# Kernel tuning notes

Hardware: AMD Instinct MI355X
Metric: run time of the kernel (lower is better)

## Reference

```python
import jax, jax.numpy as jnp
import numpy as np

BN_EPS = 1e-5
K = 3  # k_size


def _unfold(x, k):
    # torch F.unfold with padding=k//2, stride=1, viewed as (B, C, k*k, H, W).
    # Kernel positions are row-major (i slow, j fast), matching torch layout.
    p = k // 2
    B, C, H, W = x.shape
    xp = jnp.pad(x, ((0, 0), (0, 0), (p, p), (p, p)))
    pats = jnp.stack([xp[:, :, i:i + H, j:j + W]
                      for i in range(k) for j in range(k)], axis=2)
    return pats  # (B, C, k*k, H, W)


def _conv1x1(x, w, b):
    # w: (C_out, C_in), x: (B, C_in, H, W)
    return jnp.einsum('oc,bchw->bohw', w, x) + b[None, :, None, None]


def _bn(x, gamma, beta, mean, var):
    inv = gamma / jnp.sqrt(var + BN_EPS)
    return x * inv[None, :, None, None] + (beta - mean * inv)[None, :, None, None]


def setup_inputs() -> dict:
    key = jax.random.key(0)
    ks = jax.random.split(key, 12)
    B, C, H, W = 8, 256, 64, 64
    s = lambda k_, *sh: jax.random.normal(k_, sh, dtype=jnp.float32) * 0.05
    return {
        'x': jax.random.normal(ks[0], (B, C, H, W), dtype=jnp.float32),
        # feature_embedding: Conv2d(C, C, 1) + BN
        'w_embed': s(ks[1], C, C), 'b_embed': jnp.zeros((C,), jnp.float32),
        'bn1_gamma': jnp.ones((C,), jnp.float32), 'bn1_beta': jnp.zeros((C,), jnp.float32),
        'bn1_mean': jnp.zeros((C,), jnp.float32), 'bn1_var': jnp.ones((C,), jnp.float32),
        # enhance: Conv2d(2C, C, 1) + BN
        'w_enh': s(ks[2], C, 2 * C), 'b_enh': jnp.zeros((C,), jnp.float32),
        'bn2_gamma': jnp.ones((C,), jnp.float32), 'bn2_beta': jnp.zeros((C,), jnp.float32),
        'bn2_mean': jnp.zeros((C,), jnp.float32), 'bn2_var': jnp.ones((C,), jnp.float32),
        # weight_gen: Conv2d(2C, C//4, 1) -> ReLU -> Conv2d(C//4, C, 1) -> Sigmoid
        'w_g1': s(ks[3], C // 4, 2 * C), 'b_g1': jnp.zeros((C // 4,), jnp.float32),
        'w_g2': s(ks[4], C, C // 4), 'b_g2': jnp.zeros((C,), jnp.float32),
    }


def reference(x, w_embed, b_embed, bn1_gamma, bn1_beta, bn1_mean, bn1_var,
              w_enh, b_enh, bn2_gamma, bn2_beta, bn2_mean, bn2_var,
              w_g1, b_g1, w_g2, b_g2):
    B, C, H, W = x.shape
    # ---- feature embedding: 1x1 conv + BN (eval) + ReLU
    fe = jax.nn.relu(_bn(_conv1x1(x, w_embed, b_embed),
                         bn1_gamma, bn1_beta, bn1_mean, bn1_var))
    # ---- region similarity: cosine(center pixel, each kxk neighbor) over C
    pats = _unfold(fe, K)                       # (B, C, k2, H, W)
    sim = jnp.einsum('bchw,bckhw->bkhw', fe, pats)
    norm_c = jnp.sqrt(jnp.sum(fe * fe, axis=1))             # (B, H, W)
    norm_p = jnp.sqrt(jnp.sum(pats * pats, axis=1))         # (B, k2, H, W)
    sim = sim / (norm_c[:, None] * norm_p + 1e-7)
    sim = jax.nn.softmax(sim, axis=1)                       # over k2 window
    # ---- dynamic feature aggregation on original x
    xpats = _unfold(x, K)                                   # (B, C, k2, H, W)
    agg = jnp.einsum('bckhw,bkhw->bchw', xpats, sim)
    enhanced = jax.nn.relu(_bn(_conv1x1(jnp.concatenate([x, agg], axis=1), w_enh, b_enh),
                               bn2_gamma, bn2_beta, bn2_mean, bn2_var))
    # ---- output modulation (SE-style gating)
    pooled = jnp.mean(jnp.concatenate([x, enhanced], axis=1), axis=(2, 3), keepdims=True)
    h = jax.nn.relu(_conv1x1(pooled, w_g1, b_g1))
    weights = jax.nn.sigmoid(_conv1x1(h, w_g2, b_g2))       # (B, C, 1, 1)
    return x + weights * enhanced
```

## Files before the change

kernel.cpp:

```cpp
#include <hip/hip_runtime.h>
#include <math.h>

typedef unsigned short u16;
typedef unsigned int   u32;
typedef __attribute__((ext_vector_type(8))) short short8;
typedef __attribute__((ext_vector_type(4))) float f32x4;

#define HW 4096

#define OFS_XB   0ul
#define OFS_PD   8388608ul
#define OFS_W1B  8683520ul
#define OFS_W2B  8716288ul
#define OFS_B1   8781824ul
#define OFS_B2   8782080ul
#define OFS_POOL 8782336ul
#define OFS_GATE 8786432ul
#define OFS_ENH  8788480ul

__device__ __forceinline__ u16 f2bf(float x) {
    union { float f; u32 u; } v; v.f = x;
    u32 r = v.u + 0x7fffu + ((v.u >> 16) & 1u);
    return (u16)(r >> 16);
}
__device__ __forceinline__ float bf2f(u16 h) {
    union { u32 u; float f; } v; v.u = ((u32)h) << 16;
    return v.f;
}
__device__ __forceinline__ void ld_g2l_16(u16* l, const u16* g) {
    __builtin_amdgcn_global_load_lds(
        (const __attribute__((address_space(1))) u32*)g,
        (__attribute__((address_space(3))) u32*)l,
        16, 0, 0);
}

__global__ __launch_bounds__(256) void k_cvt(
    const float* __restrict__ x, u16* __restrict__ xb, float* __restrict__ pool,
    const float* __restrict__ w1, const float* __restrict__ b1,
    const float* __restrict__ g1, const float* __restrict__ be1,
    const float* __restrict__ m1, const float* __restrict__ v1,
    const float* __restrict__ w2, const float* __restrict__ b2,
    const float* __restrict__ g2, const float* __restrict__ be2,
    const float* __restrict__ m2, const float* __restrict__ v2,
    u16* __restrict__ w1b, u16* __restrict__ w2b,
    float* __restrict__ b1f, float* __restrict__ b2f,
    float* __restrict__ pd)
{
    __shared__ float tile[64][65];
    const int t = threadIdx.x;
    const int id = blockIdx.x;
    if (id < 292) {
        const float4 z = {0.f, 0.f, 0.f, 0.f};
        if (id < 288) ((float4*)(pd + id * 1024))[t] = z;
        else          ((float4*)(pool + (id - 288) * 1024))[t] = z;
        return;
    }
    if (id < 1062) {
        int idx = (id - 292) * 256 + t;
        if (idx < 65536) {
            int o = idx >> 8;
            float inv = g1[o] * rsqrtf(v1[o] + 1e-5f);
            w1b[idx] = f2bf(w1[idx] * inv);
        } else if (idx < 196608) {
            int j = idx - 65536;
            int o = j >> 9;
            float inv = g2[o] * rsqrtf(v2[o] + 1e-5f);
            w2b[j] = f2bf(w2[j] * inv);
        } else if (idx < 196864) {
            int o = idx - 196608;
            float inv = g1[o] * rsqrtf(v1[o] + 1e-5f);
            b1f[o] = b1[o] * inv + be1[o] - m1[o] * inv;
        } else if (idx < 197120) {
            int o = idx - 196864;
            float inv = g2[o] * rsqrtf(v2[o] + 1e-5f);
            b2f[o] = b2[o] * inv + be2[o] - m2[o] * inv;
        }
        return;
    }
    const int cid = id - 1062;
    const int pt = cid & 63, ct = (cid >> 6) & 3, b = cid >> 8;
    const float* src = x + (((size_t)(b * 256 + ct * 64)) << 12) + pt * 64;
#pragma unroll
    for (int i = 0; i < 16; ++i) {
        int idx = i * 256 + t;
        int cl = idx >> 6, pl = idx & 63;
        tile[cl][pl] = src[((size_t)cl << 12) + pl];
    }
    __syncthreads();
#pragma unroll
    for (int i = 0; i < 8; ++i) {
        int idx = i * 256 + t;
        int pl = idx >> 5, c2 = idx & 31;
        int cl = c2 * 2;
        u32 lo = f2bf(tile[cl][pl]);
        u32 hi = f2bf(tile[cl + 1][pl]);
        *(u32*)(xb + (((size_t)(b * 4096 + pt * 64 + pl)) << 9) + ct * 64 + cl) = lo | (hi << 16);
    }
    if (t < 64) {
        float s = 0.f;
#pragma unroll
        for (int i = 0; i < 64; ++i) s += tile[t][i];
        atomicAdd(&pool[(b << 9) + ct * 64 + t], s * (1.f / 4096.f));
    }
}

template<int KIN, bool OUTBF, bool DOPOOL>
__global__ __launch_bounds__(256) void k_gemm(
    const u16* __restrict__ xb, const u16* __restrict__ Wb,
    const float* __restrict__ biasf, void* __restrict__ outp,
    float* __restrict__ poolp)
{
    __shared__ __align__(16) u16 Wl[4096];
    __shared__ __align__(16) u16 Xl[4096];
    __shared__ float sbias[128];
    const int t = threadIdx.x;
    const int lane = t & 63;
    const int wv = t >> 6;
    const int id = blockIdx.x;
    const int p_blk = (((id >> 4) << 3) | (id & 7)) * 128;
    const int o_blk = ((id >> 3) & 1) * 128;
    const int owg = (wv & 1) * 4;
    const int pwg = (wv >> 1) * 4;
    const int r16 = lane & 15, q = lane >> 4;
    if (t < 128) sbias[t] = biasf[o_blk + t];

    f32x4 acc[4][4];
#pragma unroll
    for (int i = 0; i < 4; ++i)
#pragma unroll
        for (int j = 0; j < 4; ++j) acc[i][j] = (f32x4){0.f, 0.f, 0.f, 0.f};

    for (int kc = 0; kc < KIN / 32; ++kc) {
        const int kk = kc * 32 + q * 8;
#pragma unroll
        for (int s = 0; s < 4; ++s) {
            const int bi = wv * 4 + s;
            const u16* g;
            u16* l;
            if (bi < 8) {
                g = Wb + (size_t)(o_blk + bi * 16 + r16) * KIN + kk;
                l = Wl + bi * 512;
            } else {
                g = xb + (((size_t)(p_blk + (bi - 8) * 16 + r16)) << 9) + kk;
                l = Xl + (bi - 8) * 512;
            }
            ld_g2l_16(l, g);
        }
        __syncthreads();
        short8 af[4], bf[4];
#pragma unroll
        for (int i = 0; i < 4; ++i) af[i] = *(const short8*)(Wl + (owg + i) * 512 + lane * 8);
#pragma unroll
        for (int j = 0; j < 4; ++j) bf[j] = *(const short8*)(Xl + (pwg + j) * 512 + lane * 8);
#pragma unroll
        for (int i = 0; i < 4; ++i)
#pragma unroll
            for (int j = 0; j < 4; ++j)
                acc[i][j] = __builtin_amdgcn_mfma_f32_16x16x32_bf16(af[i], bf[j], acc[i][j], 0, 0, 0);
        __syncthreads();
    }

    float bia[4][4];
#pragma unroll
    for (int i = 0; i < 4; ++i)
#pragma unroll
        for (int r = 0; r < 4; ++r) bia[i][r] = sbias[owg * 16 + i * 16 + q * 4 + r];
    const int bidx = p_blk >> 12;
    const int pin0 = (p_blk & 4095) + pwg * 16 + r16;
#pragma unroll
    for (int i = 0; i < 4; ++i) {
#pragma unroll
        for (int r = 0; r < 4; ++r) {
            const int o = o_blk + owg * 16 + i * 16 + q * 4 + r;
            const size_t rowb = ((size_t)(bidx * 256 + o)) << 12;
            float ps = 0.f;
#pragma unroll
            for (int j = 0; j < 4; ++j) {
                float v = fmaxf(acc[i][j][r] + bia[i][r], 0.f);
                const size_t oi = rowb + pin0 + j * 16;
                ((u16*)outp)[oi] = f2bf(v);
                ps += v;
            }
            if (DOPOOL) {
                ps += __shfl_down(ps, 8, 16);
                ps += __shfl_down(ps, 4, 16);
                ps += __shfl_down(ps, 2, 16);
                ps += __shfl_down(ps, 1, 16);
                if (r16 == 0)
                    atomicAdd(&poolp[(bidx << 9) + 256 + o], ps * (1.f / 4096.f));
            }
        }
    }
}

__global__ __launch_bounds__(256) void k_sim(
    const u16* __restrict__ fe, float* __restrict__ pd)
{
    __shared__ __align__(16) u16 st[3 * 4096];
    __shared__ float red[4][64][9];
    const int t = threadIdx.x;
    const int id = blockIdx.x;
    const int b = id & 7, h = (id >> 3) & 63, g = id >> 9;
    const int rows[3] = {h > 0 ? h - 1 : 0, h, h < 63 ? h + 1 : 63};
    const u16* base = fe + (((size_t)(b * 256 + g * 64)) << 12);
#pragma unroll
    for (int it = 0; it < 6; ++it) {
        const int flat = it * 256 + t;
        const int r = flat >> 9, j = flat & 511;
        const u16* gs = base + ((size_t)(j >> 3) << 12) + rows[r] * 64 + (j & 7) * 8;
        ld_g2l_16(st + r * 4096 + j * 8, gs);
    }
    __syncthreads();
    const int w = t & 63, sl = t >> 6;
    const int wl = w > 0 ? w - 1 : 0, wr = w < 63 ? w + 1 : 63;
    float dot[9] = {};
    const u16* s0 = st + sl * 16 * 64;
#pragma unroll 4
    for (int ci = 0; ci < 16; ++ci) {
        const u16* pc = s0 + ci * 64;
        float v[9];
#pragma unroll
        for (int r = 0; r < 3; ++r) {
            v[r * 3 + 0] = bf2f(pc[r * 4096 + wl]);
            v[r * 3 + 1] = bf2f(pc[r * 4096 + w]);
            v[r * 3 + 2] = bf2f(pc[r * 4096 + wr]);
        }
        const float c0 = v[4];
#pragma unroll
        for (int k = 0; k < 9; ++k) dot[k] = fmaf(c0, v[k], dot[k]);
    }
#pragma unroll
    for (int k = 0; k < 9; ++k) red[sl][w][k] = dot[k];
    __syncthreads();
    if (t < 64) {
        const int p = h * 64 + w;
#pragma unroll
        for (int k = 0; k < 9; ++k) {
            float s = red[0][w][k] + red[1][w][k] + red[2][w][k] + red[3][w][k];
            atomicAdd(&pd[((size_t)(b * 9 + k) << 12) + p], s);
        }
    }
}

__global__ __launch_bounds__(256) void k_agg(
    const u16* __restrict__ xb, const float* __restrict__ pd,
    u16* __restrict__ xbo)
{
    __shared__ __align__(16) u16 xt[3 * 4096];
    __shared__ float ws9[9][64];
    const int t = threadIdx.x;
    const int id = blockIdx.x;
    const int b = id & 7, h = (id >> 3) & 63, g = id >> 9;
    const int rows[3] = {h > 0 ? h - 1 : 0, h, h < 63 ? h + 1 : 63};
    const u16* base = xb + (((size_t)(b * 4096)) << 9) + g * 64;
#pragma unroll
    for (int it = 0; it < 6; ++it) {
        const int flat = it * 256 + t;
        const int r = flat >> 9, j = flat & 511;
        const u16* gs = base + (((size_t)(rows[r] * 64 + (j >> 3))) << 9) + (j & 7) * 8;
        ld_g2l_16(xt + r * 4096 + j * 8, gs);
    }
    if (t < 64) {
        const int w = t;
        const int p = h * 64 + w;
        const float* pb = pd + (((size_t)(b * 9)) << 12);
        const float nc = sqrtf(pb[(4 << 12) + p]);
        float s[9], mk[9];
#pragma unroll
        for (int di = -1; di <= 1; ++di)
#pragma unroll
            for (int dj = -1; dj <= 1; ++dj) {
                const int k = (di + 1) * 3 + (dj + 1);
                const int hn = h + di, wn = w + dj;
                const float mask = (hn >= 0 && hn < 64 && wn >= 0 && wn < 64) ? 1.f : 0.f;
                const int hc = hn < 0 ? 0 : (hn > 63 ? 63 : hn);
                const int wc = wn < 0 ? 0 : (wn > 63 ? 63 : wn);
                const float nk = pb[(4 << 12) + hc * 64 + wc];
                const float dk = pb[(k << 12) + p];
                mk[k] = mask;
                s[k] = mask * dk / (nc * sqrtf(nk) + 1e-7f);
            }
        float mx = s[0];
#pragma unroll
        for (int k = 1; k < 9; ++k) mx = fmaxf(mx, s[k]);
        float e[9], sum = 0.f;
#pragma unroll
        for (int k = 0; k < 9; ++k) { e[k] = expf(s[k] - mx); sum += e[k]; }
        const float rs = 1.f / sum;
#pragma unroll
        for (int k = 0; k < 9; ++k) ws9[k][w] = mk[k] * e[k] * rs;
    }
    __syncthreads();
    const int c = t & 63, pg = t >> 6;
    u16* orow = xbo + (((size_t)(b * 4096 + h * 64)) << 9) + 256 + g * 64 + c;
#pragma unroll 4
    for (int pi = 0; pi < 16; ++pi) {
        const int px = pg * 16 + pi;
        const int pl = px > 0 ? px - 1 : 0, pr = px < 63 ? px + 1 : 63;
        const int pxs[3] = {pl, px, pr};
        float m[9];
#pragma unroll
        for (int k = 0; k < 9; ++k) m[k] = ws9[k][px];
        float acc = 0.f;
#pragma unroll
        for (int r = 0; r < 3; ++r)
#pragma unroll
            for (int j = 0; j < 3; ++j)
                acc = fmaf(bf2f(xt[r * 4096 + pxs[j] * 64 + c]), m[r * 3 + j], acc);
        orow[(size_t)px << 9] = f2bf(acc);
    }
}

__global__ __launch_bounds__(256) void k_mlp(
    const float* __restrict__ pool,
    const float* __restrict__ wg1, const float* __restrict__ bg1,
    const float* __restrict__ wg2, const float* __restrict__ bg2,
    float* __restrict__ gate)
{
    __shared__ float pl[512];
    __shared__ float hpart[4][64];
    __shared__ float hb[64];
    const int b = blockIdx.x, t = threadIdx.x;
    pl[t] = pool[b * 512 + t];
    pl[t + 256] = pool[b * 512 + t + 256];
    __syncthreads();
    const int o = t & 63, seg = t >> 6;
    float s = 0.f;
    const float* wr = wg1 + o * 512 + seg * 128;
    const float* pr = pl + seg * 128;
#pragma unroll 4
    for (int j = 0; j < 128; ++j) s = fmaf(wr[j], pr[j], s);
    hpart[seg][o] = s;
    __syncthreads();
    if (t < 64)
        hb[t] = fmaxf(hpart[0][t] + hpart[1][t] + hpart[2][t] + hpart[3][t] + bg1[t], 0.f);
    __syncthreads();
    float s2 = bg2[t];
    const float* w2 = wg2 + t * 64;
#pragma unroll 4
    for (int j = 0; j < 64; ++j) s2 = fmaf(w2[j], hb[j], s2);
    gate[b * 256 + t] = 1.f / (1.f + expf(-s2));
}

__global__ __launch_bounds__(256) void k_final(
    const u16* __restrict__ xb, const u16* __restrict__ enh,
    const float* __restrict__ gate, float* __restrict__ out)
{
    const int t = threadIdx.x;
    const int id = blockIdx.x;
    const int b = id & 7, rg = id >> 3;
    const int w = t & 63, s = t >> 6;
    const int p = rg * 64 + w;
    const u16* xrow = xb + (((size_t)(b * 4096 + p)) << 9) + s * 64;
#pragma unroll 2
    for (int cc = 0; cc < 8; ++cc) {
        short8 xv = *(const short8*)(xrow + cc * 8);
#pragma unroll
        for (int u = 0; u < 8; ++u) {
            const int c = s * 64 + cc * 8 + u;
            const float gt = gate[(b << 8) + c];
            const size_t off = (((size_t)(b * 256 + c)) << 12) + p;
            out[off] = fmaf(gt, bf2f(enh[off]), bf2f((u16)xv[u]));
        }
    }
}

extern "C" void kernel_launch(void* const* d_in, const int* in_sizes, int n_in,
                              void* d_out, int out_size, void* d_ws, size_t ws_size,
                              hipStream_t stream)
{
    const float* x       = (const float*)d_in[0];
    const float* w_embed = (const float*)d_in[1];
    const float* b_embed = (const float*)d_in[2];
    const float* g1      = (const float*)d_in[3];
    const float* be1     = (const float*)d_in[4];
    const float* m1      = (const float*)d_in[5];
    const float* v1      = (const float*)d_in[6];
    const float* w_enh   = (const float*)d_in[7];
    const float* b_enh   = (const float*)d_in[8];
    const float* g2      = (const float*)d_in[9];
    const float* be2     = (const float*)d_in[10];
    const float* m2      = (const float*)d_in[11];
    const float* v2      = (const float*)d_in[12];
    const float* w_g1    = (const float*)d_in[13];
    const float* b_g1    = (const float*)d_in[14];
    const float* w_g2    = (const float*)d_in[15];
    const float* b_g2    = (const float*)d_in[16];
    float* ws  = (float*)d_ws;
    float* out = (float*)d_out;

    u16*   xb   = (u16*)(ws + OFS_XB);
    float* pd   = ws + OFS_PD;
    u16*   w1b  = (u16*)(ws + OFS_W1B);
    u16*   w2b  = (u16*)(ws + OFS_W2B);
    float* b1f  = ws + OFS_B1;
    float* b2f  = ws + OFS_B2;
    float* pool = ws + OFS_POOL;
    float* gate = ws + OFS_GATE;
    u16*   enh  = (u16*)(ws + OFS_ENH);
    u16*   fe   = (u16*)d_out;

    k_cvt<<<dim3(3110), dim3(256), 0, stream>>>(
        x, xb, pool,
        w_embed, b_embed, g1, be1, m1, v1,
        w_enh, b_enh, g2, be2, m2, v2, w1b, w2b, b1f, b2f, pd);
    k_gemm<256, true, false><<<dim3(512), dim3(256), 0, stream>>>(xb, w1b, b1f, (void*)fe, nullptr);
    k_sim<<<dim3(2048), dim3(256), 0, stream>>>(fe, pd);
    k_agg<<<dim3(2048), dim3(256), 0, stream>>>(xb, pd, xb);
    k_gemm<512, true, true><<<dim3(512), dim3(256), 0, stream>>>(xb, w2b, b2f, (void*)enh, pool);
    k_mlp<<<dim3(8), dim3(256), 0, stream>>>(pool, w_g1, b_g1, w_g2, b_g2, gate);
    k_final<<<dim3(512), dim3(256), 0, stream>>>(xb, enh, gate, out);
}
```

Before: 203.9 us.

## Fuse similarity and aggregation into one kernel, fold gate MLP into final kernel

Merges k_sim and k_agg into one kernel where each 512-thread block handles a full image row across all 256 channels. Dot products and norms are reduced in LDS, which removes the pd atomic buffer, its zeroing and the global round trip. The same LDS buffer is then reused for the x tile in the aggregation step, which now writes channel pairs with 32-bit stores. The gate MLP is recomputed redundantly in every k_final block, dropping a launch and the gate buffer at the cost of repeated small matvecs and larger LDS use per block (lower occupancy).

```diff
diff --git a/kernel.cpp b/kernel.cpp
--- a/kernel.cpp
+++ b/kernel.cpp
@@ -6,17 +6,13 @@
 typedef __attribute__((ext_vector_type(8))) short short8;
 typedef __attribute__((ext_vector_type(4))) float f32x4;
 
-#define HW 4096
-
 #define OFS_XB   0ul
-#define OFS_PD   8388608ul
-#define OFS_W1B  8683520ul
-#define OFS_W2B  8716288ul
-#define OFS_B1   8781824ul
-#define OFS_B2   8782080ul
-#define OFS_POOL 8782336ul
-#define OFS_GATE 8786432ul
-#define OFS_ENH  8788480ul
+#define OFS_W1B  8388608ul
+#define OFS_W2B  8421376ul
+#define OFS_B1   8486912ul
+#define OFS_B2   8487168ul
+#define OFS_POOL 8487424ul
+#define OFS_ENH  8491520ul
 
 __device__ __forceinline__ u16 f2bf(float x) {
     union { float f; u32 u; } v; v.f = x;
@@ -43,20 +39,19 @@
     const float* __restrict__ g2, const float* __restrict__ be2,
     const float* __restrict__ m2, const float* __restrict__ v2,
     u16* __restrict__ w1b, u16* __restrict__ w2b,
-    float* __restrict__ b1f, float* __restrict__ b2f,
-    float* __restrict__ pd)
+    float* __restrict__ b1f, float* __restrict__ b2f)
 {
     __shared__ float tile[64][65];
     const int t = threadIdx.x;
     const int id = blockIdx.x;
-    if (id < 292) {
+    if (id < 1) {
         const float4 z = {0.f, 0.f, 0.f, 0.f};
-        if (id < 288) ((float4*)(pd + id * 1024))[t] = z;
-        else          ((float4*)(pool + (id - 288) * 1024))[t] = z;
+#pragma unroll
+        for (int i = 0; i < 4; ++i) ((float4*)pool)[i * 256 + t] = z;
         return;
     }
-    if (id < 1062) {
-        int idx = (id - 292) * 256 + t;
+    if (id < 771) {
+        int idx = (id - 1) * 256 + t;
         if (idx < 65536) {
             int o = idx >> 8;
             float inv = g1[o] * rsqrtf(v1[o] + 1e-5f);
@@ -77,7 +72,7 @@
         }
         return;
     }
-    const int cid = id - 1062;
+    const int cid = id - 771;
     const int pt = cid & 63, ct = (cid >> 6) & 3, b = cid >> 8;
     const float* src = x + (((size_t)(b * 256 + ct * 64)) << 12) + pt * 64;
 #pragma unroll
@@ -193,172 +188,180 @@
     }
 }
 
-__global__ __launch_bounds__(256) void k_sim(
-    const u16* __restrict__ fe, float* __restrict__ pd)
+__global__ __launch_bounds__(512) void k_simagg(
+    const u16* __restrict__ fe, const u16* __restrict__ xb, u16* __restrict__ xbo)
 {
-    __shared__ __align__(16) u16 st[3 * 4096];
-    __shared__ float red[4][64][9];
-    const int t = threadIdx.x;
-    const int id = blockIdx.x;
-    const int b = id & 7, h = (id >> 3) & 63, g = id >> 9;
-    const int rows[3] = {h > 0 ? h - 1 : 0, h, h < 63 ? h + 1 : 63};
-    const u16* base = fe + (((size_t)(b * 256 + g * 64)) << 12);
-#pragma unroll
-    for (int it = 0; it < 6; ++it) {
-        const int flat = it * 256 + t;
-        const int r = flat >> 9, j = flat & 511;
-        const u16* gs = base + ((size_t)(j >> 3) << 12) + rows[r] * 64 + (j & 7) * 8;
-        ld_g2l_16(st + r * 4096 + j * 8, gs);
-    }
-    __syncthreads();
-    const int w = t & 63, sl = t >> 6;
-    const int wl = w > 0 ? w - 1 : 0, wr = w < 63 ? w + 1 : 63;
-    float dot[9] = {};
-    const u16* s0 = st + sl * 16 * 64;
-#pragma unroll 4
-    for (int ci = 0; ci < 16; ++ci) {
-        const u16* pc = s0 + ci * 64;
-        float v[9];
-#pragma unroll
-        for (int r = 0; r < 3; ++r) {
-            v[r * 3 + 0] = bf2f(pc[r * 4096 + wl]);
-            v[r * 3 + 1] = bf2f(pc[r * 4096 + w]);
-            v[r * 3 + 2] = bf2f(pc[r * 4096 + wr]);
-        }
-        const float c0 = v[4];
-#pragma unroll
-        for (int k = 0; k < 9; ++k) dot[k] = fmaf(c0, v[k], dot[k]);
-    }
-#pragma unroll
-    for (int k = 0; k < 9; ++k) red[sl][w][k] = dot[k];
-    __syncthreads();
-    if (t < 64) {
-        const int p = h * 64 + w;
-#pragma unroll
-        for (int k = 0; k < 9; ++k) {
-            float s = red[0][w][k] + red[1][w][k] + red[2][w][k] + red[3][w][k];
-            atomicAdd(&pd[((size_t)(b * 9 + k) << 12) + p], s);
-        }
-    }
-}
-
-__global__ __launch_bounds__(256) void k_agg(
-    const u16* __restrict__ xb, const float* __restrict__ pd,
-    u16* __restrict__ xbo)
-{
-    __shared__ __align__(16) u16 xt[3 * 4096];
+    __shared__ __align__(16) u16 st[3 * 16384];
+    __shared__ float red[8][64][13];
     __shared__ float ws9[9][64];
     const int t = threadIdx.x;
     const int id = blockIdx.x;
-    const int b = id & 7, h = (id >> 3) & 63, g = id >> 9;
+    const int b = id & 7, h = id >> 3;
     const int rows[3] = {h > 0 ? h - 1 : 0, h, h < 63 ? h + 1 : 63};
-    const u16* base = xb + (((size_t)(b * 4096)) << 9) + g * 64;
-#pragma unroll
-    for (int it = 0; it < 6; ++it) {
-        const int flat = it * 256 + t;
-        const int r = flat >> 9, j = flat & 511;
-        const u16* gs = base + (((size_t)(rows[r] * 64 + (j >> 3))) << 9) + (j & 7) * 8;
-        ld_g2l_16(xt + r * 4096 + j * 8, gs);
+
+    {
+        const u16* base = fe + ((size_t)(b * 256) << 12);
+#pragma unroll
+        for (int it = 0; it < 12; ++it) {
+            const int flat = it * 512 + t;
+            const int r = flat >> 11, j = flat & 2047;
+            const u16* gs = base + ((size_t)(j >> 3) << 12) + rows[r] * 64 + (j & 7) * 8;
+            ld_g2l_16(st + r * 16384 + j * 8, gs);
+        }
+    }
+    __syncthreads();
+    const int w = t & 63, sl = t >> 6;
+    {
+        const int wl = w > 0 ? w - 1 : 0, wr = w < 63 ? w + 1 : 63;
+        float dot[9] = {};
+        float nn[3] = {};
+        const u16* s0 = st + sl * 2048;
+#pragma unroll 4
+        for (int ci = 0; ci < 32; ++ci) {
+            const u16* pc = s0 + ci * 64;
+            float v[9];
+#pragma unroll
+            for (int r = 0; r < 3; ++r) {
+                v[r * 3 + 0] = bf2f(pc[r * 16384 + wl]);
+                v[r * 3 + 1] = bf2f(pc[r * 16384 + w]);
+                v[r * 3 + 2] = bf2f(pc[r * 16384 + wr]);
+            }
+            const float c0 = v[4];
+#pragma unroll
+            for (int k = 0; k < 9; ++k) dot[k] = fmaf(c0, v[k], dot[k]);
+#pragma unroll
+            for (int r = 0; r < 3; ++r) nn[r] = fmaf(v[r * 3 + 1], v[r * 3 + 1], nn[r]);
+        }
+#pragma unroll
+        for (int k = 0; k < 9; ++k) red[sl][w][k] = dot[k];
+#pragma unroll
+        for (int r = 0; r < 3; ++r) red[sl][w][9 + r] = nn[r];
+    }
+    __syncthreads();
+    {
+        const u16* base = xb + ((size_t)(b * 4096) << 9);
+#pragma unroll
+        for (int it = 0; it < 12; ++it) {
+            const int flat = it * 512 + t;
+            const int r = flat >> 11, j = flat & 2047;
+            const u16* gs = base + (((size_t)(rows[r] * 64 + (j >> 5))) << 9) + (j & 31) * 8;
+            ld_g2l_16(st + r * 16384 + j * 8, gs);
+        }
     }
     if (t < 64) {
-        const int w = t;
-        const int p = h * 64 + w;
-        const float* pb = pd + (((size_t)(b * 9)) << 12);
-        const float nc = sqrtf(pb[(4 << 12) + p]);
-        float s[9], mk[9];
-#pragma unroll
-        for (int di = -1; di <= 1; ++di)
+        float dk[9], nr[3];
+#pragma unroll
+        for (int k = 0; k < 9; ++k) {
+            float s = red[0][w][k];
+#pragma unroll
+            for (int g = 1; g < 8; ++g) s += red[g][w][k];
+            dk[k] = s;
+        }
+#pragma unroll
+        for (int r = 0; r < 3; ++r) {
+            float s = red[0][w][9 + r];
+#pragma unroll
+            for (int g = 1; g < 8; ++g) s += red[g][w][9 + r];
+            nr[r] = s;
+        }
+        const float nc = sqrtf(nr[1]);
+        float sv[9], mk[9];
+#pragma unroll
+        for (int di = -1; di <= 1; ++di) {
 #pragma unroll
             for (int dj = -1; dj <= 1; ++dj) {
                 const int k = (di + 1) * 3 + (dj + 1);
                 const int hn = h + di, wn = w + dj;
                 const float mask = (hn >= 0 && hn < 64 && wn >= 0 && wn < 64) ? 1.f : 0.f;
-                const int hc = hn < 0 ? 0 : (hn > 63 ? 63 : hn);
                 const int wc = wn < 0 ? 0 : (wn > 63 ? 63 : wn);
-                const float nk = pb[(4 << 12) + hc * 64 + wc];
-                const float dk = pb[(k << 12) + p];
+                const float nk = __shfl(nr[di + 1], wc, 64);
                 mk[k] = mask;
-                s[k] = mask * dk / (nc * sqrtf(nk) + 1e-7f);
-            }
-        float mx = s[0];
-#pragma unroll
-        for (int k = 1; k < 9; ++k) mx = fmaxf(mx, s[k]);
+                sv[k] = mask * dk[k] / (nc * sqrtf(nk) + 1e-7f);
+            }
+        }
+        float mx = sv[0];
+#pragma unroll
+        for (int k = 1; k < 9; ++k) mx = fmaxf(mx, sv[k]);
         float e[9], sum = 0.f;
 #pragma unroll
-        for (int k = 0; k < 9; ++k) { e[k] = expf(s[k] - mx); sum += e[k]; }
+        for (int k = 0; k < 9; ++k) { e[k] = expf(sv[k] - mx); sum += e[k]; }
         const float rs = 1.f / sum;
 #pragma unroll
         for (int k = 0; k < 9; ++k) ws9[k][w] = mk[k] * e[k] * rs;
     }
     __syncthreads();
-    const int c = t & 63, pg = t >> 6;
-    u16* orow = xbo + (((size_t)(b * 4096 + h * 64)) << 9) + 256 + g * 64 + c;
+    const int cpair = (t & 127) * 2;
+    const int pxg = t >> 7;
+    u16* orow = xbo + (((size_t)(b * 4096 + h * 64)) << 9) + 256 + cpair;
 #pragma unroll 4
     for (int pi = 0; pi < 16; ++pi) {
-        const int px = pg * 16 + pi;
-        const int pl = px > 0 ? px - 1 : 0, pr = px < 63 ? px + 1 : 63;
-        const int pxs[3] = {pl, px, pr};
-        float m[9];
-#pragma unroll
-        for (int k = 0; k < 9; ++k) m[k] = ws9[k][px];
-        float acc = 0.f;
+        const int px = pxg * 16 + pi;
+        const int pL = px > 0 ? px - 1 : 0, pR = px < 63 ? px + 1 : 63;
+        const int pxs[3] = {pL, px, pR};
+        float m9[9];
+#pragma unroll
+        for (int k = 0; k < 9; ++k) m9[k] = ws9[k][px];
+        float a0 = 0.f, a1 = 0.f;
 #pragma unroll
         for (int r = 0; r < 3; ++r)
 #pragma unroll
-            for (int j = 0; j < 3; ++j)
-                acc = fmaf(bf2f(xt[r * 4096 + pxs[j] * 64 + c]), m[r * 3 + j], acc);
-        orow[(size_t)px << 9] = f2bf(acc);
-    }
-}
-
-__global__ __launch_bounds__(256) void k_mlp(
+            for (int j = 0; j < 3; ++j) {
+                const u32 vv = *(const u32*)(st + r * 16384 + pxs[j] * 256 + cpair);
+                a0 = fmaf(bf2f((u16)(vv & 0xffffu)), m9[r * 3 + j], a0);
+                a1 = fmaf(bf2f((u16)(vv >> 16)),     m9[r * 3 + j], a1);
+            }
+        *(u32*)(orow + ((size_t)px << 9)) = (u32)f2bf(a0) | ((u32)f2bf(a1) << 16);
+    }
+}
+
+__global__ __launch_bounds__(256) void k_final(
+    const u16* __restrict__ xb, const u16* __restrict__ enh,
     const float* __restrict__ pool,
     const float* __restrict__ wg1, const float* __restrict__ bg1,
     const float* __restrict__ wg2, const float* __restrict__ bg2,
-    float* __restrict__ gate)
+    float* __restrict__ out)
 {
     __shared__ float pl[512];
     __shared__ float hpart[4][64];
     __shared__ float hb[64];
-    const int b = blockIdx.x, t = threadIdx.x;
-    pl[t] = pool[b * 512 + t];
-    pl[t + 256] = pool[b * 512 + t + 256];
-    __syncthreads();
-    const int o = t & 63, seg = t >> 6;
-    float s = 0.f;
-    const float* wr = wg1 + o * 512 + seg * 128;
-    const float* pr = pl + seg * 128;
-#pragma unroll 4
-    for (int j = 0; j < 128; ++j) s = fmaf(wr[j], pr[j], s);
-    hpart[seg][o] = s;
-    __syncthreads();
-    if (t < 64)
-        hb[t] = fmaxf(hpart[0][t] + hpart[1][t] + hpart[2][t] + hpart[3][t] + bg1[t], 0.f);
-    __syncthreads();
-    float s2 = bg2[t];
-    const float* w2 = wg2 + t * 64;
-#pragma unroll 4
-    for (int j = 0; j < 64; ++j) s2 = fmaf(w2[j], hb[j], s2);
-    gate[b * 256 + t] = 1.f / (1.f + expf(-s2));
-}
-
-__global__ __launch_bounds__(256) void k_final(
-    const u16* __restrict__ xb, const u16* __restrict__ enh,
-    const float* __restrict__ gate, float* __restrict__ out)
-{
+    __shared__ float sg[256];
     const int t = threadIdx.x;
     const int id = blockIdx.x;
     const int b = id & 7, rg = id >> 3;
-    const int w = t & 63, s = t >> 6;
+    pl[t] = pool[b * 512 + t];
+    pl[t + 256] = pool[b * 512 + 256 + t];
+    __syncthreads();
+    {
+        const int o = t & 63, seg = t >> 6;
+        float s = 0.f;
+        const float* wr_ = wg1 + o * 512 + seg * 128;
+        const float* pr_ = pl + seg * 128;
+#pragma unroll 4
+        for (int j = 0; j < 128; ++j) s = fmaf(wr_[j], pr_[j], s);
+        hpart[seg][o] = s;
+    }
+    __syncthreads();
+    if (t < 64)
+        hb[t] = fmaxf(hpart[0][t] + hpart[1][t] + hpart[2][t] + hpart[3][t] + bg1[t], 0.f);
+    __syncthreads();
+    {
+        float s2 = bg2[t];
+        const float* w2 = wg2 + t * 64;
+#pragma unroll 4
+        for (int j = 0; j < 64; ++j) s2 = fmaf(w2[j], hb[j], s2);
+        sg[t] = 1.f / (1.f + expf(-s2));
+    }
+    __syncthreads();
+    const int w = t & 63, cs = t >> 6;
     const int p = rg * 64 + w;
-    const u16* xrow = xb + (((size_t)(b * 4096 + p)) << 9) + s * 64;
+    const u16* xrow = xb + (((size_t)(b * 4096 + p)) << 9) + cs * 64;
 #pragma unroll 2
     for (int cc = 0; cc < 8; ++cc) {
         short8 xv = *(const short8*)(xrow + cc * 8);
 #pragma unroll
         for (int u = 0; u < 8; ++u) {
-            const int c = s * 64 + cc * 8 + u;
-            const float gt = gate[(b << 8) + c];
+            const int c = cs * 64 + cc * 8 + u;
+            const float gt = sg[c];
             const size_t off = (((size_t)(b * 256 + c)) << 12) + p;
             out[off] = fmaf(gt, bf2f(enh[off]), bf2f((u16)xv[u]));
         }
@@ -390,24 +393,20 @@
     float* out = (float*)d_out;
 
     u16*   xb   = (u16*)(ws + OFS_XB);
-    float* pd   = ws + OFS_PD;
     u16*   w1b  = (u16*)(ws + OFS_W1B);
     u16*   w2b  = (u16*)(ws + OFS_W2B);
     float* b1f  = ws + OFS_B1;
     float* b2f  = ws + OFS_B2;
     float* pool = ws + OFS_POOL;
-    float* gate = ws + OFS_GATE;
     u16*   enh  = (u16*)(ws + OFS_ENH);
     u16*   fe   = (u16*)d_out;
 
-    k_cvt<<<dim3(3110), dim3(256), 0, stream>>>(
+    k_cvt<<<dim3(2819), dim3(256), 0, stream>>>(
         x, xb, pool,
         w_embed, b_embed, g1, be1, m1, v1,
-        w_enh, b_enh, g2, be2, m2, v2, w1b, w2b, b1f, b2f, pd);
+        w_enh, b_enh, g2, be2, m2, v2, w1b, w2b, b1f, b2f);
     k_gemm<256, true, false><<<dim3(512), dim3(256), 0, stream>>>(xb, w1b, b1f, (void*)fe, nullptr);
-    k_sim<<<dim3(2048), dim3(256), 0, stream>>>(fe, pd);
-    k_agg<<<dim3(2048), dim3(256), 0, stream>>>(xb, pd, xb);
+    k_simagg<<<dim3(512), dim3(512), 0, stream>>>(fe, xb, xb);
     k_gemm<512, true, true><<<dim3(512), dim3(256), 0, stream>>>(xb, w2b, b2f, (void*)enh, pool);
-    k_mlp<<<dim3(8), dim3(256), 0, stream>>>(pool, w_g1, b_g1, w_g2, b_g2, gate);
-    k_final<<<dim3(512), dim3(256), 0, stream>>>(xb, enh, gate, out);
-}
+    k_final<<<dim3(512), dim3(256), 0, stream>>>(xb, enh, pool, w_g1, b_g1, w_g2, b_g2, out);
+}
```

Measured after the change: 205.1 us. Within noise of the previous version (+0.6%).
